# Kernel optimization log

Hardware: AMD Instinct MI355X
Metric: run time of the kernel (lower is better)

## Reference

```python
import jax, jax.numpy as jnp
import numpy as np

MAP_CHANNEL_WEIGHT = 50.0
PATCH = 3  # unfold kernel size and stride (stride == kernel -> non-overlapping)


def setup_inputs() -> dict:
    key = jax.random.key(0)
    k1, k2, k3, k4 = jax.random.split(key, 4)
    style_resp = jax.random.normal(k1, (1, 256, 256, 256), dtype=jnp.float32)
    style_map = jax.random.uniform(k2, (1, 3, 1024, 1024), dtype=jnp.float32)
    output_map = jax.random.uniform(k3, (1, 3, 1024, 1024), dtype=jnp.float32)
    model_resp = jax.random.normal(k4, (1, 256, 256, 256), dtype=jnp.float32)
    return {"style_resp": style_resp, "style_map": style_map,
            "output_map": output_map, "model_resp": model_resp}


def _avg_pool(x, d):
    # x: (N, C, H, W) -> AvgPool2d((d, d)) with default stride = kernel
    n, c, h, w = x.shape
    return x.reshape(n, c, h // d, d, w // d, d).mean(axis=(3, 5))


def _unfold(x):
    # x: (C, H, W) -> (C*3*3, P) matching torch.nn.Unfold((3,3), stride=3)
    # block layout along dim 0 is (C, kh, kw); patches are row-major.
    c, h, w = x.shape
    nh = (h - PATCH) // PATCH + 1
    nw = (w - PATCH) // PATCH + 1
    x = x[:, : nh * PATCH, : nw * PATCH].reshape(c, nh, PATCH, nw, PATCH)
    x = x.transpose(0, 2, 4, 1, 3)  # (C, kh, kw, nh, nw)
    return x.reshape(c * PATCH * PATCH, nh * nw)


def reference(style_resp, style_map, output_map, model_resp):
    # --- init-time precomputation (faithful to __init__) ---
    channel_count = style_resp.shape[0]  # original code uses dim 0 (batch) here
    patch_height = style_resp.shape[2]
    down = style_map.shape[2] // patch_height
    style_map_down = _avg_pool(style_map, down)
    output_map_down = _avg_pool(output_map, down)
    sr = jnp.concatenate(
        [style_resp, MAP_CHANNEL_WEIGHT * style_map_down * channel_count], axis=1)
    style_patches = _unfold(sr[0])                      # (D, P)
    style_norm_inv = 1.0 / jnp.linalg.norm(style_patches, axis=0)  # (P,)

    # --- loss(model_response) ---
    img = jnp.concatenate(
        [model_resp, MAP_CHANNEL_WEIGHT * output_map_down * channel_count], axis=1)
    img_patches = _unfold(img[0])                       # (D, P)
    img_norm_inv = 1.0 / jnp.linalg.norm(img_patches, axis=0)      # (P,)

    # Faithful to original: sim = ((img^T @ style) * img_norm[j]).T * style_norm[j]
    # => C[i, j] = <img_j, style_i> * img_norm_inv[i] * style_norm_inv[j]
    sim = jnp.einsum('di,dj->ij', style_patches, img_patches)  # (P, P): <style_i, img_j>
    sim = sim * img_norm_inv[:, None] * style_norm_inv[None, :]
    nearest = jnp.argmax(sim, axis=1)                   # (P,)

    matched = style_patches[:, nearest]                 # (D, P)
    loss = jnp.mean((img_patches - matched) ** 2)
    return loss
```

## Files before the change

kernel.cpp:

```cpp
#include <hip/hip_runtime.h>
#include <float.h>
#include <math.h>

#define D_REAL 2331
#define D_PAD  2336
#define DQ     2304
#define N_REAL 7225
#define N_PAD  7296
#define JTILES 57
#define ITILES 57
#define STILES 15

typedef __attribute__((ext_vector_type(8))) short bf16x8_t;
typedef __attribute__((ext_vector_type(4))) float f32x4_t;
typedef __attribute__((ext_vector_type(8))) int   v8i_t;
typedef __attribute__((ext_vector_type(4))) int   v4i_t;

__device__ __forceinline__ unsigned short f2bf(float x) {
    union { float f; unsigned int u; } v; v.f = x;
    unsigned int r = v.u + 0x7FFFu + ((v.u >> 16) & 1u);
    return (unsigned short)(r >> 16);
}
__device__ __forceinline__ float bflo(unsigned int u) {
    union { unsigned int x; float f; } v; v.x = u << 16; return v.f;
}
__device__ __forceinline__ float bfhi(unsigned int u) {
    union { unsigned int x; float f; } v; v.x = u & 0xFFFF0000u; return v.f;
}

#define GLOAD_LDS16(g, l) __builtin_amdgcn_global_load_lds( \
    (const __attribute__((address_space(1))) void*)(g),     \
    (__attribute__((address_space(3))) void*)(l), 16, 0, 0)

__global__ __launch_bounds__(256) void build_all(
        const float* __restrict__ respS, const float* __restrict__ respI,
        const float* __restrict__ mapS,  const float* __restrict__ mapI,
        unsigned short* __restrict__ PbS, unsigned short* __restrict__ PbI,
        unsigned char* __restrict__ PqS, unsigned char* __restrict__ PqI) {
    const int mat = blockIdx.y;
    unsigned short* Pb = mat ? PbI : PbS;
    const int bx = blockIdx.x;
    if (bx < 6120) {
        const float* resp = mat ? respI : respS;
        unsigned char* Pq = mat ? PqI : PqS;
        __shared__ float slab[5 * 768];
        const int u  = bx / 72;
        const int d0 = (bx - u * 72) * 32;
        const int c0 = d0 / 9;
        const int cN = (d0 + 31) / 9 - c0 + 1;
        const int total = cN * 768;
        for (int idx = threadIdx.x; idx < total; idx += 256) {
            int cc = idx / 768;
            int rem = idx - cc * 768;
            slab[idx] = resp[(((size_t)(c0 + cc)) << 16) + ((size_t)(3 * u) << 8) + rem];
        }
        __syncthreads();
        const int dl16 = threadIdx.x & 15;
        const int de = d0 + 2 * dl16, dq = de + 1;
        const int ce = de / 9, re = de - ce * 9, pe = re / 3, qe = re - pe * 3;
        const int co = dq / 9, ro = dq - co * 9, po = ro / 3, qo = ro - po * 3;
        const int base_e = (ce - c0) * 768 + pe * 256 + qe;
        const int base_o = (co - c0) * 768 + po * 256 + qo;
        const int v0 = threadIdx.x >> 4;
        for (int v = v0; v < 85; v += 16) {
            float x0 = slab[base_e + 3 * v];
            float x1 = slab[base_o + 3 * v];
            size_t row = (size_t)(u * 85 + v);
            *(unsigned int*)&Pb[row * D_PAD + de] =
                (unsigned int)f2bf(x0) | ((unsigned int)f2bf(x1) << 16);
            int pk = __builtin_amdgcn_cvt_pk_fp8_f32(x0, x1, 0, false);
            *(unsigned short*)&Pq[row * DQ + de] = (unsigned short)pk;
        }
    } else {
        const float* map = mat ? mapI : mapS;
        int t = (bx - 6120) * 256 + threadIdx.x;
        int n = t >> 5, dm = t & 31;
        if (n >= N_REAL) return;
        float val = 0.f;
        if (dm < 27) {
            int u = n / 85, v = n - u * 85;
            int ch = dm / 9, r9 = dm - ch * 9, p = r9 / 3, q = r9 - p * 3;
            const float* mp = map + ((size_t)ch << 20)
                                  + ((size_t)((3 * u + p) * 4) << 10)
                                  + (size_t)((3 * v + q) * 4);
            float s = 0.f;
            #pragma unroll
            for (int a = 0; a < 4; a++)
                #pragma unroll
                for (int b = 0; b < 4; b++) s += mp[a * 1024 + b];
            val = 3.125f * s;
        }
        Pb[(size_t)n * D_PAD + 2304 + dm] = f2bf(val);
    }
}

__global__ __launch_bounds__(256) void col_norms(const unsigned short* __restrict__ Sb,
                                                 float* __restrict__ sinv,
                                                 double* __restrict__ accum) {
    if (blockIdx.x == 0 && threadIdx.x == 0) *accum = 0.0;
    int n = blockIdx.x * 4 + (threadIdx.x >> 6);
    int lane = threadIdx.x & 63;
    const uint4* sp = (const uint4*)(Sb + (size_t)n * D_PAD);
    float s = 0.f;
    for (int k = lane; k < D_PAD / 8; k += 64) {
        uint4 a = sp[k];
        float x0 = bflo(a.x), x1 = bfhi(a.x), x2 = bflo(a.y), x3 = bfhi(a.y);
        float x4 = bflo(a.z), x5 = bfhi(a.z), x6 = bflo(a.w), x7 = bfhi(a.w);
        s = fmaf(x0, x0, s); s = fmaf(x1, x1, s);
        s = fmaf(x2, x2, s); s = fmaf(x3, x3, s);
        s = fmaf(x4, x4, s); s = fmaf(x5, x5, s);
        s = fmaf(x6, x6, s); s = fmaf(x7, x7, s);
    }
    #pragma unroll
    for (int off = 32; off > 0; off >>= 1) s += __shfl_xor(s, off);
    if (lane == 0) sinv[n] = (n < N_REAL) ? rsqrtf(s) : 0.f;
}

__global__ __launch_bounds__(256) void gemm_argmax(
        const unsigned char* __restrict__ Sq, const unsigned char* __restrict__ Iq,
        const unsigned short* __restrict__ Sb, const unsigned short* __restrict__ Ib,
        const float* __restrict__ sinv,
        float* __restrict__ pval, int* __restrict__ pidx) {
    const int lb = blockIdx.x;
    const int sup = lb >> 4, win = lb & 15;
    const int it4 = (sup / STILES) * 4 + (win & 3);
    const int jt4 = (sup % STILES) * 4 + (win >> 2);
    if (it4 >= ITILES || jt4 >= JTILES) return;
    const int i0 = it4 * 128, j0 = jt4 * 128;

    __shared__ __align__(16) unsigned char Af[2][128][128];
    __shared__ __align__(16) unsigned char Bf[2][128][128];
    const int tid = threadIdx.x;
    const int L = tid & 63, w = tid >> 6;
    const int m = L & 15, q = L >> 4;
    const int wi = (w >> 1) * 64, wj = (w & 1) * 64;

    f32x4_t acc[4][4];
    #pragma unroll
    for (int a = 0; a < 4; a++)
        #pragma unroll
        for (int b = 0; b < 4; b++) acc[a][b] = (f32x4_t){0.f, 0.f, 0.f, 0.f};

    const int rl = L >> 3;
    const int ck = (L & 7) ^ rl;
    const unsigned char* gqa = Sq + (size_t)(i0 + w * 32 + rl) * DQ + (ck << 4);
    const unsigned char* gqb = Iq + (size_t)(j0 + w * 32 + rl) * DQ + (ck << 4);

    const int clo = ((((q << 1))     ^ (m & 7)) << 4);
    const int chi = ((((q << 1) | 1) ^ (m & 7)) << 4);

    unsigned short (*At)[32] = (unsigned short(*)[32])&Af[0][0][0];
    unsigned short (*Bt)[32] = (unsigned short(*)[32])&Bf[0][0][0];
    const int rl2 = L >> 2;
    const int ck2 = (L & 3) ^ ((rl2 >> 1) & 3);
    const unsigned short* gta = Sb + (size_t)(i0 + w * 32 + rl2) * D_PAD + 2304 + (ck2 << 3);
    const unsigned short* gtb = Ib + (size_t)(j0 + w * 32 + rl2) * D_PAD + 2304 + (ck2 << 3);
    const int cht = (q ^ ((m >> 1) & 3)) << 3;

#define PREFETCH_Q(buf) {                                     \
    GLOAD_LDS16(gqa,             &Af[buf][w * 32     ][0]);   \
    GLOAD_LDS16(gqa +  8 * DQ,   &Af[buf][w * 32 +  8][0]);   \
    GLOAD_LDS16(gqa + 16 * DQ,   &Af[buf][w * 32 + 16][0]);   \
    GLOAD_LDS16(gqa + 24 * DQ,   &Af[buf][w * 32 + 24][0]);   \
    GLOAD_LDS16(gqb,             &Bf[buf][w * 32     ][0]);   \
    GLOAD_LDS16(gqb +  8 * DQ,   &Bf[buf][w * 32 +  8][0]);   \
    GLOAD_LDS16(gqb + 16 * DQ,   &Bf[buf][w * 32 + 16][0]);   \
    GLOAD_LDS16(gqb + 24 * DQ,   &Bf[buf][w * 32 + 24][0]);   \
    gqa += 128; gqb += 128; }

#define COMPUTE_Q(buf) {                                                   \
    v8i_t aq[4], bq[4];                                                    \
    _Pragma("unroll")                                                      \
    for (int mi = 0; mi < 4; mi++) {                                       \
        v4i_t lo = *(const v4i_t*)&Af[buf][wi + mi * 16 + m][clo];         \
        v4i_t hi = *(const v4i_t*)&Af[buf][wi + mi * 16 + m][chi];         \
        aq[mi] = __builtin_shufflevector(lo, hi, 0, 1, 2, 3, 4, 5, 6, 7);  \
    }                                                                      \
    _Pragma("unroll")                                                      \
    for (int nj = 0; nj < 4; nj++) {                                       \
        v4i_t lo = *(const v4i_t*)&Bf[buf][wj + nj * 16 + m][clo];         \
        v4i_t hi = *(const v4i_t*)&Bf[buf][wj + nj * 16 + m][chi];         \
        bq[nj] = __builtin_shufflevector(lo, hi, 0, 1, 2, 3, 4, 5, 6, 7);  \
    }                                                                      \
    _Pragma("unroll")                                                      \
    for (int mi = 0; mi < 4; mi++)                                         \
        _Pragma("unroll")                                                  \
        for (int nj = 0; nj < 4; nj++)                                     \
            acc[mi][nj] = __builtin_amdgcn_mfma_scale_f32_16x16x128_f8f6f4(\
                aq[mi], bq[nj], acc[mi][nj], 0, 0, 0, 0x7F, 0, 0x7F); }

    PREFETCH_Q(0)
    for (int p = 0; p < 8; p++) {
        __syncthreads();
        PREFETCH_Q(1)
        __builtin_amdgcn_sched_barrier(0);
        COMPUTE_Q(0)
        __syncthreads();
        PREFETCH_Q(0)
        __builtin_amdgcn_sched_barrier(0);
        COMPUTE_Q(1)
    }
    __syncthreads();
    PREFETCH_Q(1)
    __builtin_amdgcn_sched_barrier(0);
    COMPUTE_Q(0)
    __syncthreads();
    {
        GLOAD_LDS16(gta,                      &At[w * 32][0]);
        GLOAD_LDS16(gta + (size_t)16 * D_PAD, &At[w * 32 + 16][0]);
        GLOAD_LDS16(gtb,                      &Bt[w * 32][0]);
        GLOAD_LDS16(gtb + (size_t)16 * D_PAD, &Bt[w * 32 + 16][0]);
    }
    __builtin_amdgcn_sched_barrier(0);
    COMPUTE_Q(1)
    __syncthreads();
    {
        bf16x8_t af[4], bfr[4];
        #pragma unroll
        for (int mi = 0; mi < 4; mi++)
            af[mi] = *(const bf16x8_t*)&At[wi + mi * 16 + m][cht];
        #pragma unroll
        for (int nj = 0; nj < 4; nj++)
            bfr[nj] = *(const bf16x8_t*)&Bt[wj + nj * 16 + m][cht];
        #pragma unroll
        for (int mi = 0; mi < 4; mi++)
            #pragma unroll
            for (int nj = 0; nj < 4; nj++)
                acc[mi][nj] = __builtin_amdgcn_mfma_f32_16x16x32_bf16(
                    af[mi], bfr[nj], acc[mi][nj], 0, 0, 0);
    }
#undef PREFETCH_Q
#undef COMPUTE_Q

    float sjv[4];
    #pragma unroll
    for (int nj = 0; nj < 4; nj++) sjv[nj] = sinv[j0 + wj + nj * 16 + m];
    #pragma unroll
    for (int mi = 0; mi < 4; mi++) {
        #pragma unroll
        for (int r = 0; r < 4; r++) {
            float best = -INFINITY; int bidx = 0x7fffffff;
            #pragma unroll
            for (int nj = 0; nj < 4; nj++) {
                int j = j0 + wj + nj * 16 + m;
                float v = (j < N_REAL) ? acc[mi][nj][r] * sjv[nj] : -INFINITY;
                if (v > best) { best = v; bidx = j; }
            }
            #pragma unroll
            for (int off = 1; off < 16; off <<= 1) {
                float ov = __shfl_xor(best, off);
                int   oi = __shfl_xor(bidx, off);
                if (ov > best || (ov == best && oi < bidx)) { best = ov; bidx = oi; }
            }
            if (m == 0) {
                int i = i0 + wi + mi * 16 + q * 4 + r;
                pval[(size_t)jt4 * N_PAD + i] = best;
                pidx[(size_t)jt4 * N_PAD + i] = bidx;
            }
        }
    }
}

__global__ __launch_bounds__(256) void loss_kernel(
        const unsigned short* __restrict__ Ib, const unsigned short* __restrict__ Sb,
        const float* __restrict__ pval, const int* __restrict__ pidx,
        double* __restrict__ accum) {
    __shared__ float wsum[4];
    __shared__ int sjn;
    const int n = blockIdx.x;
    if (threadIdx.x < 64) {
        float v = -INFINITY; int id = 0x7fffffff;
        if (threadIdx.x < JTILES) {
            v  = pval[(size_t)threadIdx.x * N_PAD + n];
            id = pidx[(size_t)threadIdx.x * N_PAD + n];
        }
        #pragma unroll
        for (int off = 32; off > 0; off >>= 1) {
            float ov = __shfl_xor(v, off);
            int   oi = __shfl_xor(id, off);
            if (ov > v || (ov == v && oi < id)) { v = ov; id = oi; }
        }
        if (threadIdx.x == 0) sjn = id;
    }
    __syncthreads();
    const int jn = sjn;
    const uint4* ip = (const uint4*)(Ib + (size_t)n  * D_PAD);
    const uint4* sp = (const uint4*)(Sb + (size_t)jn * D_PAD);
    float s = 0.f;
    for (int k = threadIdx.x; k < D_PAD / 8; k += 256) {
        uint4 a = ip[k], b = sp[k];
        float d0 = bflo(a.x) - bflo(b.x), d1 = bfhi(a.x) - bfhi(b.x);
        float d2 = bflo(a.y) - bflo(b.y), d3 = bfhi(a.y) - bfhi(b.y);
        float d4 = bflo(a.z) - bflo(b.z), d5 = bfhi(a.z) - bfhi(b.z);
        float d6 = bflo(a.w) - bflo(b.w), d7 = bfhi(a.w) - bfhi(b.w);
        s = fmaf(d0, d0, s); s = fmaf(d1, d1, s);
        s = fmaf(d2, d2, s); s = fmaf(d3, d3, s);
        s = fmaf(d4, d4, s); s = fmaf(d5, d5, s);
        s = fmaf(d6, d6, s); s = fmaf(d7, d7, s);
    }
    #pragma unroll
    for (int off = 32; off > 0; off >>= 1) s += __shfl_xor(s, off);
    int lane = threadIdx.x & 63, wv = threadIdx.x >> 6;
    if (lane == 0) wsum[wv] = s;
    __syncthreads();
    if (threadIdx.x == 0) {
        double t = (double)wsum[0] + (double)wsum[1] + (double)wsum[2] + (double)wsum[3];
        atomicAdd(accum, t);
    }
}

__global__ void finalize(const double* __restrict__ accum, float* __restrict__ out) {
    out[0] = (float)(accum[0] / (double)((long long)D_REAL * N_REAL));
}

extern "C" void kernel_launch(void* const* d_in, const int* in_sizes, int n_in,
                              void* d_out, int out_size, void* d_ws, size_t ws_size,
                              hipStream_t stream) {
    const float* style_resp = (const float*)d_in[0];
    const float* style_map  = (const float*)d_in[1];
    const float* output_map = (const float*)d_in[2];
    const float* model_resp = (const float*)d_in[3];
    float* out = (float*)d_out;

    unsigned short* Sb = (unsigned short*)d_ws;
    unsigned short* Ib = Sb + (size_t)D_PAD * N_PAD;
    unsigned char*  Sq = (unsigned char*)(Ib + (size_t)D_PAD * N_PAD);
    unsigned char*  Iq = Sq + (size_t)DQ * N_PAD;
    float* sinv    = (float*)(Iq + (size_t)DQ * N_PAD);
    float* pval    = sinv + N_PAD;
    int*   pidx    = (int*)(pval + (size_t)JTILES * N_PAD);
    double* accum  = (double*)(pidx + (size_t)JTILES * N_PAD);

    build_all<<<dim3(6120 + 904, 2), 256, 0, stream>>>(
        style_resp, model_resp, style_map, output_map, Sb, Ib, Sq, Iq);

    col_norms<<<N_PAD / 4, 256, 0, stream>>>(Sb, sinv, accum);

    gemm_argmax<<<STILES * STILES * 16, 256, 0, stream>>>(Sq, Iq, Sb, Ib, sinv, pval, pidx);

    loss_kernel<<<N_REAL, 256, 0, stream>>>(Ib, Sb, pval, pidx, accum);
    finalize<<<1, 1, 0, stream>>>(accum, out);
}
```

Baseline: 491.8 us.

## Enlarge GEMM-argmax tiles to 256x256 with 8 waves and phased pipelined staging

Each workgroup of the fused fp8 GEMM plus argmax now covers a 256x256 output tile with 512 threads in a 2x4 wave grid, replacing the 128x128, 4-wave layout. The K loop is split into fine-grained phases. Each phase issues the next global-to-LDS stage, syncs with raw s_barrier and explicit waitcnt, and runs its MFMAs at raised priority so loads overlap compute. The goal is more operand reuse per byte fetched and fewer partial argmax columns for the loss kernel to reduce. The cost is about 128KB of LDS per block, heavy register use for the 8x4 accumulators, and a coarser grid with more padding in N_PAD.

```diff
diff --git a/kernel.cpp b/kernel.cpp
--- a/kernel.cpp
+++ b/kernel.cpp
@@ -6,10 +6,8 @@
 #define D_PAD  2336
 #define DQ     2304
 #define N_REAL 7225
-#define N_PAD  7296
-#define JTILES 57
-#define ITILES 57
-#define STILES 15
+#define N_PAD  7424
+#define NT     29
 
 typedef __attribute__((ext_vector_type(8))) short bf16x8_t;
 typedef __attribute__((ext_vector_type(4))) float f32x4_t;
@@ -116,133 +114,159 @@
     if (lane == 0) sinv[n] = (n < N_REAL) ? rsqrtf(s) : 0.f;
 }
 
-__global__ __launch_bounds__(256) void gemm_argmax(
+__global__ __launch_bounds__(512, 2) void gemm_argmax(
         const unsigned char* __restrict__ Sq, const unsigned char* __restrict__ Iq,
         const unsigned short* __restrict__ Sb, const unsigned short* __restrict__ Ib,
         const float* __restrict__ sinv,
         float* __restrict__ pval, int* __restrict__ pidx) {
-    const int lb = blockIdx.x;
-    const int sup = lb >> 4, win = lb & 15;
-    const int it4 = (sup / STILES) * 4 + (win & 3);
-    const int jt4 = (sup % STILES) * 4 + (win >> 2);
-    if (it4 >= ITILES || jt4 >= JTILES) return;
-    const int i0 = it4 * 128, j0 = jt4 * 128;
-
-    __shared__ __align__(16) unsigned char Af[2][128][128];
-    __shared__ __align__(16) unsigned char Bf[2][128][128];
+    const int bid = blockIdx.x;
+    const int it = bid % NT, jt = bid / NT;
+    const int i0 = it * 256, j0 = jt * 256;
+
+    __shared__ __align__(16) unsigned char Af[2][256][128];
+    __shared__ __align__(16) unsigned char Bf[2][256][128];
+
     const int tid = threadIdx.x;
     const int L = tid & 63, w = tid >> 6;
+    const int wr = w >> 2, wc = w & 3;
     const int m = L & 15, q = L >> 4;
-    const int wi = (w >> 1) * 64, wj = (w & 1) * 64;
-
-    f32x4_t acc[4][4];
-    #pragma unroll
-    for (int a = 0; a < 4; a++)
+    const int clo = ((2 * q)     ^ (m & 7)) << 4;
+    const int chi = ((2 * q + 1) ^ (m & 7)) << 4;
+
+    f32x4_t acc[8][4];
+    #pragma unroll
+    for (int a = 0; a < 8; a++)
         #pragma unroll
         for (int b = 0; b < 4; b++) acc[a][b] = (f32x4_t){0.f, 0.f, 0.f, 0.f};
 
-    const int rl = L >> 3;
-    const int ck = (L & 7) ^ rl;
-    const unsigned char* gqa = Sq + (size_t)(i0 + w * 32 + rl) * DQ + (ck << 4);
-    const unsigned char* gqb = Iq + (size_t)(j0 + w * 32 + rl) * DQ + (ck << 4);
-
-    const int clo = ((((q << 1))     ^ (m & 7)) << 4);
-    const int chi = ((((q << 1) | 1) ^ (m & 7)) << 4);
+    const int aro = 128 * (w >> 2) + 8 * (w & 3);
+    const int bro = 8 * w;
+    const unsigned char* pA = Sq + (size_t)(i0 + aro + (L >> 3)) * DQ
+                            + (((L & 7) ^ (L >> 3)) << 4);
+    const unsigned char* pB = Iq + (size_t)(j0 + bro + (L >> 3)) * DQ
+                            + (((L & 7) ^ (L >> 3)) << 4);
+
+#define STG_A(s, ko, b) GLOAD_LDS16(pA + (size_t)(32 * (s)) * DQ + (ko), \
+                                    &Af[b][32 * (s) + aro][0])
+#define STG_B(s, ko, b) GLOAD_LDS16(pB + (size_t)(64 * (s)) * DQ + (ko), \
+                                    &Bf[b][64 * (s) + bro][0])
+
+#define LDA8(dst, b, mi) {                                              \
+    const unsigned char* p_ = &Af[b][wr * 128 + (mi) * 16 + m][0];      \
+    v4i_t lo_ = *(const v4i_t*)(p_ + clo);                              \
+    v4i_t hi_ = *(const v4i_t*)(p_ + chi);                              \
+    dst = __builtin_shufflevector(lo_, hi_, 0, 1, 2, 3, 4, 5, 6, 7); }
+#define LDB8(dst, b, nj) {                                              \
+    const unsigned char* p_ = &Bf[b][wc * 64 + (nj) * 16 + m][0];       \
+    v4i_t lo_ = *(const v4i_t*)(p_ + clo);                              \
+    v4i_t hi_ = *(const v4i_t*)(p_ + chi);                              \
+    dst = __builtin_shufflevector(lo_, hi_, 0, 1, 2, 3, 4, 5, 6, 7); }
+
+#define RDB4(b) LDB8(bq0, b, 0) LDB8(bq1, b, 1) LDB8(bq2, b, 2) LDB8(bq3, b, 3)
+
+#define MXMFMA(a, b, c) __builtin_amdgcn_mfma_scale_f32_16x16x128_f8f6f4( \
+    a, b, c, 0, 0, 0, 0x7F, 0, 0x7F)
+
+#define PHASE(b, p2, RDB, STAGES, TAILW) {                              \
+    v8i_t a0_, a1_;                                                     \
+    RDB                                                                 \
+    LDA8(a0_, b, 2 * (p2))                                              \
+    LDA8(a1_, b, 2 * (p2) + 1)                                          \
+    STAGES                                                              \
+    __builtin_amdgcn_sched_barrier(0);                                  \
+    __builtin_amdgcn_s_barrier();                                       \
+    asm volatile("s_waitcnt lgkmcnt(0)" ::: "memory");                  \
+    __builtin_amdgcn_sched_barrier(0);                                  \
+    __builtin_amdgcn_s_setprio(1);                                      \
+    acc[2*(p2)  ][0] = MXMFMA(a0_, bq0, acc[2*(p2)  ][0]);              \
+    acc[2*(p2)  ][1] = MXMFMA(a0_, bq1, acc[2*(p2)  ][1]);              \
+    acc[2*(p2)  ][2] = MXMFMA(a0_, bq2, acc[2*(p2)  ][2]);              \
+    acc[2*(p2)  ][3] = MXMFMA(a0_, bq3, acc[2*(p2)  ][3]);              \
+    acc[2*(p2)+1][0] = MXMFMA(a1_, bq0, acc[2*(p2)+1][0]);              \
+    acc[2*(p2)+1][1] = MXMFMA(a1_, bq1, acc[2*(p2)+1][1]);              \
+    acc[2*(p2)+1][2] = MXMFMA(a1_, bq2, acc[2*(p2)+1][2]);              \
+    acc[2*(p2)+1][3] = MXMFMA(a1_, bq3, acc[2*(p2)+1][3]);              \
+    __builtin_amdgcn_s_setprio(0);                                      \
+    __builtin_amdgcn_sched_barrier(0);                                  \
+    TAILW                                                               \
+    __builtin_amdgcn_s_barrier();                                       \
+}
+
+    v8i_t bq0, bq1, bq2, bq3;
+
+    STG_B(0, 0, 0); STG_A(0, 0, 0);
+    STG_B(1, 0, 0); STG_A(1, 0, 0);
+    STG_B(2, 0, 0); STG_A(2, 0, 0);
+    STG_B(3, 0, 0); STG_A(3, 0, 0);
+    STG_B(0, 128, 1); STG_A(0, 128, 1);
+    STG_B(1, 128, 1); STG_A(1, 128, 1);
+    STG_B(2, 128, 1); STG_A(2, 128, 1);
+    asm volatile("s_waitcnt vmcnt(6)" ::: "memory");
+    __builtin_amdgcn_s_barrier();
+
+    #pragma unroll 1
+    for (int i8 = 0; i8 < 8; ++i8) {
+        PHASE(0, 0, RDB4(0), STG_B(3, 128, 1); STG_A(3, 128, 1);, )
+        PHASE(0, 1, ,        STG_B(0, 256, 0); STG_A(0, 256, 0);, )
+        PHASE(0, 2, ,        STG_B(1, 256, 0); STG_A(1, 256, 0);, )
+        PHASE(0, 3, ,        STG_B(2, 256, 0); STG_A(2, 256, 0);,
+              asm volatile("s_waitcnt vmcnt(6)" ::: "memory");)
+        PHASE(1, 0, RDB4(1), STG_B(3, 256, 0); STG_A(3, 256, 0);, )
+        PHASE(1, 1, ,        STG_B(0, 384, 1); STG_A(0, 384, 1);, )
+        PHASE(1, 2, ,        STG_B(1, 384, 1); STG_A(1, 384, 1);, )
+        PHASE(1, 3, ,        STG_B(2, 384, 1); STG_A(2, 384, 1);,
+              asm volatile("s_waitcnt vmcnt(6)" ::: "memory");)
+        pA += 256; pB += 256;
+    }
 
     unsigned short (*At)[32] = (unsigned short(*)[32])&Af[0][0][0];
     unsigned short (*Bt)[32] = (unsigned short(*)[32])&Bf[0][0][0];
-    const int rl2 = L >> 2;
-    const int ck2 = (L & 3) ^ ((rl2 >> 1) & 3);
-    const unsigned short* gta = Sb + (size_t)(i0 + w * 32 + rl2) * D_PAD + 2304 + (ck2 << 3);
-    const unsigned short* gtb = Ib + (size_t)(j0 + w * 32 + rl2) * D_PAD + 2304 + (ck2 << 3);
-    const int cht = (q ^ ((m >> 1) & 3)) << 3;
-
-#define PREFETCH_Q(buf) {                                     \
-    GLOAD_LDS16(gqa,             &Af[buf][w * 32     ][0]);   \
-    GLOAD_LDS16(gqa +  8 * DQ,   &Af[buf][w * 32 +  8][0]);   \
-    GLOAD_LDS16(gqa + 16 * DQ,   &Af[buf][w * 32 + 16][0]);   \
-    GLOAD_LDS16(gqa + 24 * DQ,   &Af[buf][w * 32 + 24][0]);   \
-    GLOAD_LDS16(gqb,             &Bf[buf][w * 32     ][0]);   \
-    GLOAD_LDS16(gqb +  8 * DQ,   &Bf[buf][w * 32 +  8][0]);   \
-    GLOAD_LDS16(gqb + 16 * DQ,   &Bf[buf][w * 32 + 16][0]);   \
-    GLOAD_LDS16(gqb + 24 * DQ,   &Bf[buf][w * 32 + 24][0]);   \
-    gqa += 128; gqb += 128; }
-
-#define COMPUTE_Q(buf) {                                                   \
-    v8i_t aq[4], bq[4];                                                    \
-    _Pragma("unroll")                                                      \
-    for (int mi = 0; mi < 4; mi++) {                                       \
-        v4i_t lo = *(const v4i_t*)&Af[buf][wi + mi * 16 + m][clo];         \
-        v4i_t hi = *(const v4i_t*)&Af[buf][wi + mi * 16 + m][chi];         \
-        aq[mi] = __builtin_shufflevector(lo, hi, 0, 1, 2, 3, 4, 5, 6, 7);  \
-    }                                                                      \
-    _Pragma("unroll")                                                      \
-    for (int nj = 0; nj < 4; nj++) {                                       \
-        v4i_t lo = *(const v4i_t*)&Bf[buf][wj + nj * 16 + m][clo];         \
-        v4i_t hi = *(const v4i_t*)&Bf[buf][wj + nj * 16 + m][chi];         \
-        bq[nj] = __builtin_shufflevector(lo, hi, 0, 1, 2, 3, 4, 5, 6, 7);  \
-    }                                                                      \
-    _Pragma("unroll")                                                      \
-    for (int mi = 0; mi < 4; mi++)                                         \
-        _Pragma("unroll")                                                  \
-        for (int nj = 0; nj < 4; nj++)                                     \
-            acc[mi][nj] = __builtin_amdgcn_mfma_scale_f32_16x16x128_f8f6f4(\
-                aq[mi], bq[nj], acc[mi][nj], 0, 0, 0, 0x7F, 0, 0x7F); }
-
-    PREFETCH_Q(0)
-    for (int p = 0; p < 8; p++) {
-        __syncthreads();
-        PREFETCH_Q(1)
-        __builtin_amdgcn_sched_barrier(0);
-        COMPUTE_Q(0)
-        __syncthreads();
-        PREFETCH_Q(0)
-        __builtin_amdgcn_sched_barrier(0);
-        COMPUTE_Q(1)
-    }
-    __syncthreads();
-    PREFETCH_Q(1)
-    __builtin_amdgcn_sched_barrier(0);
-    COMPUTE_Q(0)
-    __syncthreads();
+    const unsigned short* ptA = Sb + (size_t)(i0 + 16 * w + (L >> 2)) * D_PAD
+                              + 2304 + (((L & 3) ^ ((L >> 3) & 3)) << 3);
+    const unsigned short* ptB = Ib + (size_t)(j0 + 16 * w + (L >> 2)) * D_PAD
+                              + 2304 + (((L & 3) ^ ((L >> 3) & 3)) << 3);
+
+    PHASE(0, 0, RDB4(0), STG_B(3, 128, 1); STG_A(3, 128, 1);, )
+    PHASE(0, 1, , , )
+    PHASE(0, 2, , , )
+    PHASE(0, 3, , , asm volatile("s_waitcnt vmcnt(0)" ::: "memory");)
+    PHASE(1, 0, RDB4(1), GLOAD_LDS16(ptA, &At[16 * w][0]);, )
+    PHASE(1, 1, , GLOAD_LDS16(ptA + (size_t)128 * D_PAD, &At[128 + 16 * w][0]);, )
+    PHASE(1, 2, , GLOAD_LDS16(ptB, &Bt[16 * w][0]);, )
+    PHASE(1, 3, , GLOAD_LDS16(ptB + (size_t)128 * D_PAD, &Bt[128 + 16 * w][0]);,
+          asm volatile("s_waitcnt vmcnt(0)" ::: "memory");)
+#undef PHASE
+#undef RDB4
+#undef STG_A
+#undef STG_B
+
     {
-        GLOAD_LDS16(gta,                      &At[w * 32][0]);
-        GLOAD_LDS16(gta + (size_t)16 * D_PAD, &At[w * 32 + 16][0]);
-        GLOAD_LDS16(gtb,                      &Bt[w * 32][0]);
-        GLOAD_LDS16(gtb + (size_t)16 * D_PAD, &Bt[w * 32 + 16][0]);
-    }
-    __builtin_amdgcn_sched_barrier(0);
-    COMPUTE_Q(1)
-    __syncthreads();
-    {
-        bf16x8_t af[4], bfr[4];
-        #pragma unroll
-        for (int mi = 0; mi < 4; mi++)
-            af[mi] = *(const bf16x8_t*)&At[wi + mi * 16 + m][cht];
+        const int cht = (q ^ ((m >> 1) & 3)) << 3;
+        bf16x8_t bt[4];
         #pragma unroll
         for (int nj = 0; nj < 4; nj++)
-            bfr[nj] = *(const bf16x8_t*)&Bt[wj + nj * 16 + m][cht];
-        #pragma unroll
-        for (int mi = 0; mi < 4; mi++)
+            bt[nj] = *(const bf16x8_t*)&Bt[wc * 64 + nj * 16 + m][cht];
+        #pragma unroll
+        for (int mi = 0; mi < 8; mi++) {
+            bf16x8_t a_ = *(const bf16x8_t*)&At[wr * 128 + mi * 16 + m][cht];
             #pragma unroll
             for (int nj = 0; nj < 4; nj++)
                 acc[mi][nj] = __builtin_amdgcn_mfma_f32_16x16x32_bf16(
-                    af[mi], bfr[nj], acc[mi][nj], 0, 0, 0);
-    }
-#undef PREFETCH_Q
-#undef COMPUTE_Q
+                    a_, bt[nj], acc[mi][nj], 0, 0, 0);
+        }
+    }
 
     float sjv[4];
     #pragma unroll
-    for (int nj = 0; nj < 4; nj++) sjv[nj] = sinv[j0 + wj + nj * 16 + m];
-    #pragma unroll
-    for (int mi = 0; mi < 4; mi++) {
+    for (int nj = 0; nj < 4; nj++) sjv[nj] = sinv[j0 + wc * 64 + nj * 16 + m];
+    #pragma unroll
+    for (int mi = 0; mi < 8; mi++) {
         #pragma unroll
         for (int r = 0; r < 4; r++) {
             float best = -INFINITY; int bidx = 0x7fffffff;
             #pragma unroll
             for (int nj = 0; nj < 4; nj++) {
-                int j = j0 + wj + nj * 16 + m;
+                int j = j0 + wc * 64 + nj * 16 + m;
                 float v = (j < N_REAL) ? acc[mi][nj][r] * sjv[nj] : -INFINITY;
                 if (v > best) { best = v; bidx = j; }
             }
@@ -253,9 +277,9 @@
                 if (ov > best || (ov == best && oi < bidx)) { best = ov; bidx = oi; }
             }
             if (m == 0) {
-                int i = i0 + wi + mi * 16 + q * 4 + r;
-                pval[(size_t)jt4 * N_PAD + i] = best;
-                pidx[(size_t)jt4 * N_PAD + i] = bidx;
+                int i = i0 + wr * 128 + mi * 16 + q * 4 + r;
+                pval[(size_t)jt * N_PAD + i] = best;
+                pidx[(size_t)jt * N_PAD + i] = bidx;
             }
         }
     }
@@ -270,7 +294,7 @@
     const int n = blockIdx.x;
     if (threadIdx.x < 64) {
         float v = -INFINITY; int id = 0x7fffffff;
-        if (threadIdx.x < JTILES) {
+        if (threadIdx.x < NT) {
             v  = pval[(size_t)threadIdx.x * N_PAD + n];
             id = pidx[(size_t)threadIdx.x * N_PAD + n];
         }
@@ -328,15 +352,15 @@
     unsigned char*  Iq = Sq + (size_t)DQ * N_PAD;
     float* sinv    = (float*)(Iq + (size_t)DQ * N_PAD);
     float* pval    = sinv + N_PAD;
-    int*   pidx    = (int*)(pval + (size_t)JTILES * N_PAD);
-    double* accum  = (double*)(pidx + (size_t)JTILES * N_PAD);
+    int*   pidx    = (int*)(pval + (size_t)NT * N_PAD);
+    double* accum  = (double*)(pidx + (size_t)NT * N_PAD);
 
     build_all<<<dim3(6120 + 904, 2), 256, 0, stream>>>(
         style_resp, model_resp, style_map, output_map, Sb, Ib, Sq, Iq);
 
     col_norms<<<N_PAD / 4, 256, 0, stream>>>(Sb, sinv, accum);
 
-    gemm_argmax<<<STILES * STILES * 16, 256, 0, stream>>>(Sq, Iq, Sb, Ib, sinv, pval, pidx);
+    gemm_argmax<<<NT * NT, 512, 0, stream>>>(Sq, Iq, Sb, Ib, sinv, pval, pidx);
 
     loss_kernel<<<N_REAL, 256, 0, stream>>>(Ib, Sb, pval, pidx, accum);
     finalize<<<1, 1, 0, stream>>>(accum, out);
```

Measured after the change: 501.4 us. No clear change (+2.0%).
